# Performance work log

Measured on AMD Instinct MI355X. Metric: run time of the kernel, lower is better.

Reference implementation:

```python
import jax, jax.numpy as jnp
import numpy as np

H, DK, NF, DC, B, T = 8, 64, 512, 256, 8, 1024

def setup_inputs() -> dict:
    key = jax.random.key(0)
    ks = jax.random.split(key, 16)
    s = lambda fan_in: 1.0 / np.sqrt(fan_in)
    return {
        "x": jax.random.normal(ks[0], (B, T, NF), jnp.float32),
        "cond": jax.random.normal(ks[1], (B, T, DC), jnp.float32),
        "pos_k": jax.random.normal(ks[2], (T, T, DK), jnp.float32),
        "mask": jax.random.randint(ks[3], (B, T, T), 0, 2, jnp.int32),
        "ln_gamma": jnp.ones((NF,), jnp.float32),
        "ln_beta": jnp.zeros((NF,), jnp.float32),
        "Wq": jax.random.uniform(ks[4], (NF, NF), jnp.float32, -s(NF), s(NF)),
        "bq": jax.random.uniform(ks[5], (NF,), jnp.float32, -s(NF), s(NF)),
        "Wk": jax.random.uniform(ks[6], (NF, NF), jnp.float32, -s(NF), s(NF)),
        "bk": jax.random.uniform(ks[7], (NF,), jnp.float32, -s(NF), s(NF)),
        "Wv": jax.random.uniform(ks[8], (NF, NF), jnp.float32, -s(NF), s(NF)),
        "bv": jax.random.uniform(ks[9], (NF,), jnp.float32, -s(NF), s(NF)),
        "Wo": jax.random.uniform(ks[10], (NF, NF), jnp.float32, -s(NF), s(NF)),
        "bo": jax.random.uniform(ks[11], (NF,), jnp.float32, -s(NF), s(NF)),
        "Wc": jax.random.uniform(ks[12], (DC, NF), jnp.float32, -s(DC), s(DC)),
        "bc": jax.random.uniform(ks[13], (NF,), jnp.float32, -s(DC), s(DC)),
    }

def reference(x, cond, pos_k, mask, ln_gamma, ln_beta, Wq, bq, Wk, bk, Wv, bv, Wo, bo, Wc, bc):
    # LayerNorm over features (eps matches torch default)
    mu = jnp.mean(x, axis=-1, keepdims=True)
    var = jnp.mean(jnp.square(x - mu), axis=-1, keepdims=True)
    xn = (x - mu) * jax.lax.rsqrt(var + 1e-5) * ln_gamma + ln_beta
    # projections; query comes from conditioning signal
    q = ((cond @ Wc + bc) @ Wq + bq).reshape(B, T, H, DK)
    k = (xn @ Wk + bk).reshape(B, T, H, DK)
    v = (xn @ Wv + bv).reshape(B, T, H, DK)
    # content scores + relative-position bias (matmul-trick equivalent)
    A = jnp.einsum('bthd,bshd->bhts', q, k)
    Bbias = jnp.einsum('bthd,tsd->bhts', q, pos_k)
    scores = (A + Bbias) / np.sqrt(DK)
    m0 = (mask == 0)[:, None, :, :]  # (B,1,T,T) True where masked
    min_val = jnp.finfo(scores.dtype).min
    scores = jnp.where(m0, min_val, scores)
    attn = jnp.where(m0, 0.0, jax.nn.softmax(scores, axis=-1))
    out = jnp.einsum('bhts,bshd->bthd', attn, v).reshape(B, T, NF)
    return out @ Wo + bo
```

## Files before the change

### kernel.cpp

```cpp
#include <hip/hip_runtime.h>

#define Bb 8
#define Tt 1024
#define Hh 8
#define DKk 64
#define NFf 512
#define DCc 256

typedef _Float16 v2h __attribute__((ext_vector_type(2)));
typedef _Float16 v4h __attribute__((ext_vector_type(4)));
typedef _Float16 v8h __attribute__((ext_vector_type(8)));
typedef float    v4f __attribute__((ext_vector_type(4)));
typedef float    v16f __attribute__((ext_vector_type(16)));

#define MFMA32(a,b,c) __builtin_amdgcn_mfma_f32_16x16x32_f16((a),(b),(c),0,0,0)
#define MFMA3216(a,b,c) __builtin_amdgcn_mfma_f32_32x32x16_f16((a),(b),(c),0,0,0)

#define SCQ 0.1803368801111f

__device__ inline void st8(_Float16* dst, v8h x){
    *(v4h*)dst     = __builtin_shufflevector(x,x,0,1,2,3);
    *(v4h*)(dst+4) = __builtin_shufflevector(x,x,4,5,6,7);
}

__device__ inline v8h cvt8(float4 a, float4 b){
    v8h r;
    r[0]=(_Float16)a.x; r[1]=(_Float16)a.y; r[2]=(_Float16)a.z; r[3]=(_Float16)a.w;
    r[4]=(_Float16)b.x; r[5]=(_Float16)b.y; r[6]=(_Float16)b.z; r[7]=(_Float16)b.w;
    return r;
}

__device__ inline int swz(int r, int c){ return (r*64 + c) ^ ((r&7)<<3); }

__global__ __launch_bounds__(256) void k_ln(const float* __restrict__ x,
                                            const float* __restrict__ g,
                                            const float* __restrict__ be,
                                            _Float16* __restrict__ xn){
    int row = blockIdx.x; int tid = threadIdx.x;
    const float* xr = x + (size_t)row*512;
    float2 v = reinterpret_cast<const float2*>(xr)[tid];
    float s = v.x + v.y, sq = v.x*v.x + v.y*v.y;
    for (int off=32; off; off>>=1){ s += __shfl_down(s, off); sq += __shfl_down(sq, off); }
    __shared__ float ws_[4], wq_[4];
    __shared__ float mu_s, rs_s;
    int wid = tid>>6, lid = tid&63;
    if (lid==0){ ws_[wid]=s; wq_[wid]=sq; }
    __syncthreads();
    if (tid==0){
        float S=0,Q=0;
        for(int i=0;i<4;i++){S+=ws_[i];Q+=wq_[i];}
        float mu = S*(1.f/512.f);
        float var = Q*(1.f/512.f)-mu*mu;
        mu_s=mu; rs_s=rsqrtf(var+1e-5f);
    }
    __syncthreads();
    float mu=mu_s, rs=rs_s;
    float2 gv = reinterpret_cast<const float2*>(g)[tid];
    float2 bv = reinterpret_cast<const float2*>(be)[tid];
    v2h o; o[0] = (_Float16)((v.x-mu)*rs*gv.x + bv.x);
           o[1] = (_Float16)((v.y-mu)*rs*gv.y + bv.y);
    reinterpret_cast<v2h*>(xn + (size_t)row*512)[tid] = o;
}

__global__ __launch_bounds__(256) void k_wT4(const float* __restrict__ W0,
                                             const float* __restrict__ W1,
                                             const float* __restrict__ W2,
                                             const float* __restrict__ W3,
                                             _Float16* __restrict__ T0,
                                             _Float16* __restrict__ T1,
                                             _Float16* __restrict__ T2,
                                             _Float16* __restrict__ T3){
    const float* W = (blockIdx.z==0)?W0:(blockIdx.z==1)?W1:(blockIdx.z==2)?W2:W3;
    _Float16*  WT = (blockIdx.z==0)?T0:(blockIdx.z==1)?T1:(blockIdx.z==2)?T2:T3;
    __shared__ float tile[64][65];
    int bx = blockIdx.x*64, by = blockIdx.y*64;
    int tid = threadIdx.x, c = tid&63;
    for (int r = tid>>6; r<64; r+=4) tile[r][c] = W[(size_t)(by+r)*512 + bx + c];
    __syncthreads();
    for (int n = tid>>6; n<64; n+=4) WT[(size_t)(bx+n)*512 + by + c] = (_Float16)tile[c][n];
}

__global__ __launch_bounds__(256) void k_h16(const float* __restrict__ src,
                                             _Float16* __restrict__ dst){
    int i = (blockIdx.x*256 + threadIdx.x)*8;
    float4 a = *(const float4*)(src+i);
    float4 b = *(const float4*)(src+i+4);
    *(v8h*)(dst+i) = cvt8(a,b);
}

__global__ __launch_bounds__(512) void k_bcqp(const float* __restrict__ bc,
                                              const float* __restrict__ Wq,
                                              float* __restrict__ bcq){
    int j = threadIdx.x; int m0 = blockIdx.x*16;
    float a = 0.f;
    #pragma unroll
    for (int m=0;m<16;m++) a += bc[m0+m]*Wq[(size_t)(m0+m)*512 + j];
    atomicAdd(&bcq[j], a);
}

template<typename AT, typename CT, bool QB>
__global__ __launch_bounds__(512) void k_gemm(const AT* __restrict__ A,
                                              const _Float16* __restrict__ WT,
                                              const float* __restrict__ bias,
                                              CT* __restrict__ C,
                                              int M, int N, int K,
                                              float scale,
                                              _Float16* __restrict__ qbT){
    __shared__ _Float16 Al[2][128*64];
    __shared__ _Float16 Wl[2][128*64];
    int tid = threadIdx.x, l = tid&63, w = tid>>6;
    int l15 = l&15, lq = l>>4;
    int wr = w>>2, wc = w&3;
    int m0 = blockIdx.y*128, n0 = blockIdx.x*128;
    v4f acc[4][2] = {};
    float bv[2];
    #pragma unroll
    for (int bc=0;bc<2;++bc) bv[bc] = bias[n0 + wc*32 + bc*16 + l15];
    int srow = tid>>2, sseg = (tid&3)*16;
    const AT* arow = A + (size_t)(m0+srow)*K + sseg;
    const _Float16* wrow = WT + (size_t)(n0+srow)*K + sseg;
    int NT = K>>6;

    v8h pa0, pa1, pw0, pw1;
    if constexpr (sizeof(AT)==4){
        const float* s = (const float*)arow;
        pa0 = cvt8(*(const float4*)s,     *(const float4*)(s+4));
        pa1 = cvt8(*(const float4*)(s+8), *(const float4*)(s+12));
    } else {
        pa0 = *(const v8h*)arow; pa1 = *(const v8h*)(arow+8);
    }
    pw0 = *(const v8h*)wrow; pw1 = *(const v8h*)(wrow+8);
    st8(&Al[0][swz(srow,sseg)], pa0); st8(&Al[0][swz(srow,sseg+8)], pa1);
    st8(&Wl[0][swz(srow,sseg)], pw0); st8(&Wl[0][swz(srow,sseg+8)], pw1);
    __syncthreads();

    for (int kt=0; kt<NT; ++kt){
        int cur = kt&1;
        if (kt < NT-1){
            int k0 = (kt+1)<<6;
            if constexpr (sizeof(AT)==4){
                const float* s = (const float*)arow + k0;
                pa0 = cvt8(*(const float4*)s,     *(const float4*)(s+4));
                pa1 = cvt8(*(const float4*)(s+8), *(const float4*)(s+12));
            } else {
                pa0 = *(const v8h*)(arow + k0); pa1 = *(const v8h*)(arow + k0 + 8);
            }
            pw0 = *(const v8h*)(wrow + k0); pw1 = *(const v8h*)(wrow + k0 + 8);
        }
        #pragma unroll
        for (int kk=0; kk<2; ++kk){
            v8h af[4], bf[2];
            #pragma unroll
            for (int ar=0;ar<4;++ar) af[ar] = *(v8h*)&Al[cur][swz(wr*64+ar*16+l15, kk*32+lq*8)];
            #pragma unroll
            for (int bc=0;bc<2;++bc) bf[bc] = *(v8h*)&Wl[cur][swz(wc*32+bc*16+l15, kk*32+lq*8)];
            #pragma unroll
            for (int ar=0;ar<4;++ar)
                #pragma unroll
                for (int bc=0;bc<2;++bc)
                    acc[ar][bc] = MFMA32(af[ar], bf[bc], acc[ar][bc]);
        }
        if (kt < NT-1){
            st8(&Al[cur^1][swz(srow,sseg)], pa0); st8(&Al[cur^1][swz(srow,sseg+8)], pa1);
            st8(&Wl[cur^1][swz(srow,sseg)], pw0); st8(&Wl[cur^1][swz(srow,sseg+8)], pw1);
        }
        __syncthreads();
    }
    #pragma unroll
    for (int ar=0;ar<4;++ar){
        #pragma unroll
        for (int bc=0;bc<2;++bc){
            #pragma unroll
            for (int i=0;i<4;++i){
                int row = m0 + wr*64 + ar*16 + lq*4 + i;
                int col = n0 + wc*32 + bc*16 + l15;
                float vf = (acc[ar][bc][i] + bv[bc])*scale;
                C[(size_t)row*N + col] = (CT)vf;
                if constexpr (QB){
                    int bI = row>>10, t = row&1023;
                    qbT[((size_t)t<<12) + (bI<<9) + col] = (_Float16)vf;
                }
            }
        }
    }
}

__global__ __launch_bounds__(512) void k_gemmkv(const _Float16* __restrict__ A,
                                                const _Float16* __restrict__ WTk,
                                                const _Float16* __restrict__ WTv,
                                                const float* __restrict__ bk,
                                                const float* __restrict__ bv,
                                                _Float16* __restrict__ Ck,
                                                _Float16* __restrict__ Cv){
    __shared__ _Float16 Al[2][128*64];
    __shared__ _Float16 Wkl[2][128*64];
    __shared__ _Float16 Wvl[2][128*64];
    int tid = threadIdx.x, l = tid&63, w = tid>>6;
    int l15 = l&15, lq = l>>4;
    int wr = w>>2, wc = w&3;
    int m0 = blockIdx.y*128, n0 = blockIdx.x*128;
    v4f ack[4][2] = {}, acv[4][2] = {};
    float bkr[2], bvr[2];
    #pragma unroll
    for (int bc=0;bc<2;++bc){ bkr[bc] = bk[n0 + wc*32 + bc*16 + l15]; bvr[bc] = bv[n0 + wc*32 + bc*16 + l15]; }
    int srow = tid>>2, sseg = (tid&3)*16;
    const _Float16* arow = A   + (size_t)(m0+srow)*512 + sseg;
    const _Float16* krow = WTk + (size_t)(n0+srow)*512 + sseg;
    const _Float16* vrow = WTv + (size_t)(n0+srow)*512 + sseg;

    v8h pa0,pa1,pk0,pk1,pv0,pv1;
    pa0 = *(const v8h*)arow; pa1 = *(const v8h*)(arow+8);
    pk0 = *(const v8h*)krow; pk1 = *(const v8h*)(krow+8);
    pv0 = *(const v8h*)vrow; pv1 = *(const v8h*)(vrow+8);
    st8(&Al[0][swz(srow,sseg)],  pa0); st8(&Al[0][swz(srow,sseg+8)],  pa1);
    st8(&Wkl[0][swz(srow,sseg)], pk0); st8(&Wkl[0][swz(srow,sseg+8)], pk1);
    st8(&Wvl[0][swz(srow,sseg)], pv0); st8(&Wvl[0][swz(srow,sseg+8)], pv1);
    __syncthreads();

    for (int kt=0; kt<8; ++kt){
        int cur = kt&1;
        if (kt < 7){
            int k0 = (kt+1)<<6;
            pa0 = *(const v8h*)(arow+k0); pa1 = *(const v8h*)(arow+k0+8);
            pk0 = *(const v8h*)(krow+k0); pk1 = *(const v8h*)(krow+k0+8);
            pv0 = *(const v8h*)(vrow+k0); pv1 = *(const v8h*)(vrow+k0+8);
        }
        #pragma unroll
        for (int kk=0; kk<2; ++kk){
            v8h af[4], kf[2], vf[2];
            #pragma unroll
            for (int ar=0;ar<4;++ar) af[ar] = *(v8h*)&Al[cur][swz(wr*64+ar*16+l15, kk*32+lq*8)];
            #pragma unroll
            for (int bc=0;bc<2;++bc){
                kf[bc] = *(v8h*)&Wkl[cur][swz(wc*32+bc*16+l15, kk*32+lq*8)];
                vf[bc] = *(v8h*)&Wvl[cur][swz(wc*32+bc*16+l15, kk*32+lq*8)];
            }
            #pragma unroll
            for (int ar=0;ar<4;++ar)
                #pragma unroll
                for (int bc=0;bc<2;++bc){
                    ack[ar][bc] = MFMA32(af[ar], kf[bc], ack[ar][bc]);
                    acv[ar][bc] = MFMA32(af[ar], vf[bc], acv[ar][bc]);
                }
        }
        if (kt < 7){
            st8(&Al[cur^1][swz(srow,sseg)],  pa0); st8(&Al[cur^1][swz(srow,sseg+8)],  pa1);
            st8(&Wkl[cur^1][swz(srow,sseg)], pk0); st8(&Wkl[cur^1][swz(srow,sseg+8)], pk1);
            st8(&Wvl[cur^1][swz(srow,sseg)], pv0); st8(&Wvl[cur^1][swz(srow,sseg+8)], pv1);
        }
        __syncthreads();
    }
    #pragma unroll
    for (int ar=0;ar<4;++ar){
        #pragma unroll
        for (int bc=0;bc<2;++bc){
            #pragma unroll
            for (int i=0;i<4;++i){
                int row = m0 + wr*64 + ar*16 + lq*4 + i;
                int col = n0 + wc*32 + bc*16 + l15;
                Ck[(size_t)row*512 + col] = (_Float16)(ack[ar][bc][i] + bkr[bc]);
                Cv[(size_t)row*512 + col] = (_Float16)(acv[ar][bc][i] + bvr[bc]);
            }
        }
    }
}

__global__ __launch_bounds__(256) void k_bias(const _Float16* __restrict__ qb,
                                              const float* __restrict__ posk,
                                              const int* __restrict__ mask,
                                              _Float16* __restrict__ Sb){
    __shared__ _Float16 Pl[2][64*64];
    __shared__ _Float16 Ol[2][64*72];
    int t = blockIdx.x >> 1, sh = blockIdx.x & 1;
    int tid = threadIdx.x, l = tid&63, w = tid>>6;
    int l31 = l&31, hi = l>>5;
    int g = w & 1, sg = w >> 1;
    v8h aa[4];
    const _Float16* qbt = qb + ((size_t)t<<12);
    #pragma unroll
    for (int k0=0;k0<4;++k0)
        aa[k0] = *(const v8h*)(qbt + (g*32 + l31)*64 + k0*16 + hi*8);

    const float* pkt = posk + ((size_t)t<<16);
    int sbase = sh*512;
    int lrow = (l>>4), lcol = (l&15)*4;

    v4f pf[4];
    #pragma unroll
    for (int j=0;j<4;++j)
        pf[j] = *(const v4f*)(pkt + (size_t)(sbase + w*16 + j*4 + lrow)*64 + lcol);

    int obh = tid>>2;
    int osl = (tid&3)*16;
    int ob  = obh>>3;
    const int* mbase = mask + (((size_t)(ob*Tt + t))<<10);
    _Float16* sbb = Sb + (((size_t)(t*64 + obh))<<10);

    #pragma unroll
    for (int j=0;j<4;++j){
        v4h hv; hv[0]=(_Float16)pf[j][0]; hv[1]=(_Float16)pf[j][1];
                hv[2]=(_Float16)pf[j][2]; hv[3]=(_Float16)pf[j][3];
        *(v4h*)&Pl[0][swz(w*16 + j*4 + lrow, lcol)] = hv;
    }
    __syncthreads();

    for (int sc=0; sc<8; ++sc){
        int cur = sc&1;
        int s0 = sbase + sc*64;
        if (sc < 7){
            #pragma unroll
            for (int j=0;j<4;++j)
                pf[j] = *(const v4f*)(pkt + (size_t)(s0 + 64 + w*16 + j*4 + lrow)*64 + lcol);
        }
        int4 mq[4];
        #pragma unroll
        for (int j=0;j<4;++j)
            mq[j] = *(const int4*)(mbase + s0 + osl + j*4);
        v8h bfr[4];
        #pragma unroll
        for (int k0=0;k0<4;++k0)
            bfr[k0] = *(v8h*)&Pl[cur][swz(sg*32 + l31, k0*16 + hi*8)];
        v16f acc = {};
        #pragma unroll
        for (int k0=0;k0<4;++k0) acc = MFMA3216(aa[k0], bfr[k0], acc);
        #pragma unroll
        for (int r=0;r<16;++r){
            int bh = g*32 + (r&3) + 4*hi + 8*(r>>2);
            Ol[cur][bh*72 + sg*32 + l31] = (_Float16)acc[r];
        }
        if (sc < 7){
            #pragma unroll
            for (int j=0;j<4;++j){
                v4h hv; hv[0]=(_Float16)pf[j][0]; hv[1]=(_Float16)pf[j][1];
                        hv[2]=(_Float16)pf[j][2]; hv[3]=(_Float16)pf[j][3];
                *(v4h*)&Pl[cur^1][swz(w*16 + j*4 + lrow, lcol)] = hv;
            }
        }
        __syncthreads();
        v8h o0 = *(v8h*)&Ol[cur][obh*72 + osl];
        v8h o1 = *(v8h*)&Ol[cur][obh*72 + osl + 8];
        const _Float16 NEG = (_Float16)(-30000.f);
        int mm[16] = {mq[0].x,mq[0].y,mq[0].z,mq[0].w, mq[1].x,mq[1].y,mq[1].z,mq[1].w,
                      mq[2].x,mq[2].y,mq[2].z,mq[2].w, mq[3].x,mq[3].y,mq[3].z,mq[3].w};
        #pragma unroll
        for (int j=0;j<8;++j){ if(!mm[j]) o0[j]=NEG; if(!mm[8+j]) o1[j]=NEG; }
        *(v8h*)(sbb + s0 + osl)     = o0;
        *(v8h*)(sbb + s0 + osl + 8) = o1;
    }
}

__global__ __launch_bounds__(512) void k_flash(const _Float16* __restrict__ qs,
                                               const _Float16* __restrict__ kbuf,
                                               const _Float16* __restrict__ vbuf,
                                               const _Float16* __restrict__ Sb,
                                               _Float16* __restrict__ ao){
    __shared__ _Float16 Kl[64*64];
    __shared__ _Float16 Vt[64*64];
    __shared__ _Float16 Bl[128*64];
    int bh = blockIdx.x; int b = bh>>3, h = bh&7;
    int t0 = blockIdx.y*128;
    int tid = threadIdx.x, l = tid&63, w = tid>>6, l15 = l&15, lq = l>>4;

    v8h qa[2];
    #pragma unroll
    for (int u=0;u<2;++u)
        qa[u] = *(const v8h*)(qs + ((size_t)(b*Tt + t0 + w*16 + l15))*NFf + h*DKk + u*32 + lq*8);

    v4f O[4] = {};
    float m_l = -1e30f, l_l = 0.f;

    int kr = tid>>3, kseg = (tid&7)*8;
    int vs = tid&63, vd0 = (tid>>6)*8;
    int br = tid>>2, bhf = (tid&3)*16;
    const _Float16* kbase = kbuf + ((size_t)(b*Tt + kr))*NFf + h*DKk + kseg;
    const _Float16* vbase = vbuf + ((size_t)(b*Tt + vs))*NFf + h*DKk + vd0;
    const _Float16* bbase = Sb + (((size_t)((t0+br)*64 + bh))<<10) + bhf;

    v8h pk = *(const v8h*)kbase;
    v8h pv = *(const v8h*)vbase;
    v8h pb0 = *(const v8h*)bbase;
    v8h pb1 = *((const v8h*)bbase + 1);

    for (int sc=0; sc<16; ++sc){
        st8(&Kl[swz(kr, kseg)], pk);
        #pragma unroll
        for (int j=0;j<8;j++) Vt[swz(vd0+j, vs)] = pv[j];
        st8(&Bl[swz(br, bhf)],   pb0);
        st8(&Bl[swz(br, bhf+8)], pb1);
        __syncthreads();
        if (sc < 15){
            size_t soff = (size_t)(sc+1)*64;
            pk  = *(const v8h*)(kbase + soff*NFf);
            pv  = *(const v8h*)(vbase + soff*NFf);
            pb0 = *(const v8h*)(bbase + soff);
            pb1 = *((const v8h*)(bbase + soff) + 1);
        }

        v4f sv[4];
        #pragma unroll
        for (int nt=0; nt<4; ++nt){
            v8h kb0 = *(v8h*)&Kl[swz(nt*16+l15, lq*8)];
            v8h kb1 = *(v8h*)&Kl[swz(nt*16+l15, 32+lq*8)];
            v4f a = {};
            a = MFMA32(kb0, qa[0], a);
            a = MFMA32(kb1, qa[1], a);
            v4h bl4 = *(v4h*)&Bl[swz(w*16 + l15, nt*16 + lq*4)];
            #pragma unroll
            for (int i=0;i<4;i++) a[i] += (float)bl4[i];
            sv[nt] = a;
        }
        float mx = fmaxf(fmaxf(fmaxf(sv[0][0],sv[0][1]),fmaxf(sv[0][2],sv[0][3])),
                   fmaxf(fmaxf(fmaxf(sv[1][0],sv[1][1]),fmaxf(sv[1][2],sv[1][3])),
                   fmaxf(fmaxf(fmaxf(sv[2][0],sv[2][1]),fmaxf(sv[2][2],sv[2][3])),
                         fmaxf(fmaxf(sv[3][0],sv[3][1]),fmaxf(sv[3][2],sv[3][3])))));
        mx = fmaxf(mx, __shfl_xor(mx,16));
        mx = fmaxf(mx, __shfl_xor(mx,32));
        float mn = fmaxf(m_l, mx);
        if (__any(mn - m_l > 0.f)){
            float rsc = exp2f(m_l - mn);
            m_l = mn; l_l *= rsc;
            float rscB[4];
            #pragma unroll
            for (int i=0;i<4;i++) rscB[i] = __shfl(rsc, lq*4+i);
            #pragma unroll
            for (int nt=0; nt<4; ++nt)
                #pragma unroll
                for (int i=0;i<4;i++) O[nt][i] *= rscB[i];
        }
        float ps = 0.f;
        #pragma unroll
        for (int nt=0; nt<4; ++nt){
            v4h ph;
            #pragma unroll
            for (int i=0;i<4;i++){
                float p = exp2f(sv[nt][i] - m_l);
                ph[i] = (_Float16)p;
                ps += p;
            }
            *(v4h*)&Bl[swz(w*16 + l15, nt*16 + lq*4)] = ph;
        }
        ps += __shfl_xor(ps,16);
        ps += __shfl_xor(ps,32);
        l_l += ps;
        {
            v8h pa0 = *(v8h*)&Bl[swz(w*16+l15, lq*8)];
            v8h pa1 = *(v8h*)&Bl[swz(w*16+l15, 32+lq*8)];
            #pragma unroll
            for (int nt=0; nt<4; ++nt){
                v8h vb0 = *(v8h*)&Vt[swz(nt*16+l15, lq*8)];
                v8h vb1 = *(v8h*)&Vt[swz(nt*16+l15, 32+lq*8)];
                O[nt] = MFMA32(pa0, vb0, O[nt]);
                O[nt] = MFMA32(pa1, vb1, O[nt]);
            }
        }
        __syncthreads();
    }

    float rl = (l_l > 0.f) ? 1.f/l_l : 0.f;
    float rlB[4];
    #pragma unroll
    for (int i=0;i<4;i++) rlB[i] = __shfl(rl, lq*4+i);
    #pragma unroll
    for (int i=0;i<4;i++){
        int row = t0 + w*16 + lq*4 + i;
        #pragma unroll
        for (int nt=0; nt<4; ++nt)
            ao[((size_t)(b*Tt + row))*NFf + h*DKk + nt*16 + l15] = (_Float16)(O[nt][i]*rlB[i]);
    }
}

extern "C" void kernel_launch(void* const* d_in, const int* in_sizes, int n_in,
                              void* d_out, int out_size, void* d_ws, size_t ws_size,
                              hipStream_t stream) {
    const float* x       = (const float*)d_in[0];
    const float* cond    = (const float*)d_in[1];
    const float* pos_k   = (const float*)d_in[2];
    const int*   mask    = (const int*)  d_in[3];
    const float* ln_g    = (const float*)d_in[4];
    const float* ln_b    = (const float*)d_in[5];
    const float* Wq      = (const float*)d_in[6];
    const float* bq      = (const float*)d_in[7];
    const float* Wk      = (const float*)d_in[8];
    const float* bk      = (const float*)d_in[9];
    const float* Wv      = (const float*)d_in[10];
    const float* bv      = (const float*)d_in[11];
    const float* Wo      = (const float*)d_in[12];
    const float* bo      = (const float*)d_in[13];
    const float* Wc      = (const float*)d_in[14];
    const float* bc      = (const float*)d_in[15];
    float* out = (float*)d_out;

    char* base = (char*)d_ws;
    const size_t OFF_S    = 0;
    const size_t OFF_XN   = 134217728;
    const size_t OFF_Q    = OFF_XN  + 8388608;
    const size_t OFF_QB   = OFF_Q   + 8388608;
    const size_t OFF_K    = OFF_QB  + 8388608;
    const size_t OFF_V    = OFF_K   + 8388608;
    const size_t OFF_AO   = OFF_V   + 8388608;
    const size_t OFF_WKT  = OFF_AO  + 8388608;
    const size_t OFF_WVT  = OFF_WKT + 524288;
    const size_t OFF_WOT  = OFF_WVT + 524288;
    const size_t OFF_WQT  = OFF_WOT + 524288;
    const size_t OFF_WCH  = OFF_WQT + 524288;
    const size_t OFF_WCQT = OFF_WCH + 262144;
    const size_t OFF_BCQ  = OFF_WCQT + 262144;
    const size_t OFF_ZERO = OFF_BCQ + 2048;

    _Float16* xn    = (_Float16*)(base + OFF_XN);
    _Float16* qbuf  = (_Float16*)(base + OFF_Q);
    _Float16* qb    = (_Float16*)(base + OFF_QB);
    _Float16* kb    = (_Float16*)(base + OFF_K);
    _Float16* vb    = (_Float16*)(base + OFF_V);
    _Float16* ao    = (_Float16*)(base + OFF_AO);
    _Float16* Sb    = (_Float16*)(base + OFF_S);
    _Float16* WkT   = (_Float16*)(base + OFF_WKT);
    _Float16* WvT   = (_Float16*)(base + OFF_WVT);
    _Float16* WoT   = (_Float16*)(base + OFF_WOT);
    _Float16* WqT   = (_Float16*)(base + OFF_WQT);
    _Float16* WcH   = (_Float16*)(base + OFF_WCH);
    _Float16* wcqT  = (_Float16*)(base + OFF_WCQT);
    float*    bcq   = (float*)(base + OFF_BCQ);
    float*    zero  = (float*)(base + OFF_ZERO);

    hipMemsetAsync(zero, 0, 1024, stream);
    hipMemcpyAsync(bcq, bq, 2048, hipMemcpyDeviceToDevice, stream);

    k_ln<<<dim3(Bb*Tt), dim3(256), 0, stream>>>(x, ln_g, ln_b, xn);
    k_wT4<<<dim3(8,8,4), dim3(256), 0, stream>>>(Wk, Wv, Wo, Wq, WkT, WvT, WoT, WqT);
    k_h16<<<dim3(64), dim3(256), 0, stream>>>(Wc, WcH);
    k_bcqp<<<dim3(16), dim3(512), 0, stream>>>(bc, Wq, bcq);

    k_gemm<_Float16,_Float16,false><<<dim3(2,4), dim3(512), 0, stream>>>(WqT, WcH, zero, wcqT, 512, 256, 512, 1.f, nullptr);

    k_gemm<float,_Float16,true><<<dim3(4,64), dim3(512), 0, stream>>>(cond, wcqT, bcq, qbuf, Bb*Tt, 512, 256, SCQ, qb);
    k_gemmkv<<<dim3(4,64), dim3(512), 0, stream>>>(xn, WkT, WvT, bk, bv, kb, vb);

    k_bias<<<dim3(2048), dim3(256), 0, stream>>>(qb, pos_k, mask, Sb);
    k_flash<<<dim3(64,8), dim3(512), 0, stream>>>(qbuf, kb, vb, Sb, ao);

    k_gemm<_Float16,float,false><<<dim3(4,64), dim3(512), 0, stream>>>(ao, WoT, bo, out, Bb*Tt, 512, 512, 1.f, nullptr);
}
```

Baseline: 225.1 us.

## Double-buffer flash attention LDS tiles and fuse weight prep kernels

Flash attention now keeps two LDS buffers for the K, V and bias tiles. The next tile is stored into the alternate buffer after the PV MFMAs, so each iteration needs one barrier instead of two. Weight transposes, the Wc fp16 conversion, the zero buffer init and the bias copy are merged into one prep kernel, replacing the separate memset/memcpy calls and extra launches. In exchange the attention kernel's shared memory use doubles, which may lower occupancy.

```diff
diff --git a/kernel.cpp b/kernel.cpp
--- a/kernel.cpp
+++ b/kernel.cpp
@@ -62,30 +62,39 @@
     reinterpret_cast<v2h*>(xn + (size_t)row*512)[tid] = o;
 }
 
-__global__ __launch_bounds__(256) void k_wT4(const float* __restrict__ W0,
-                                             const float* __restrict__ W1,
-                                             const float* __restrict__ W2,
-                                             const float* __restrict__ W3,
-                                             _Float16* __restrict__ T0,
-                                             _Float16* __restrict__ T1,
-                                             _Float16* __restrict__ T2,
-                                             _Float16* __restrict__ T3){
-    const float* W = (blockIdx.z==0)?W0:(blockIdx.z==1)?W1:(blockIdx.z==2)?W2:W3;
-    _Float16*  WT = (blockIdx.z==0)?T0:(blockIdx.z==1)?T1:(blockIdx.z==2)?T2:T3;
+__global__ __launch_bounds__(256) void k_prep(const float* __restrict__ Wk,
+                                              const float* __restrict__ Wv,
+                                              const float* __restrict__ Wo,
+                                              const float* __restrict__ Wq,
+                                              _Float16* __restrict__ WkT,
+                                              _Float16* __restrict__ WvT,
+                                              _Float16* __restrict__ WoT,
+                                              _Float16* __restrict__ WqT,
+                                              const float* __restrict__ Wc,
+                                              _Float16* __restrict__ WcH,
+                                              const float* __restrict__ bq,
+                                              float* __restrict__ bcq,
+                                              float* __restrict__ zero){
     __shared__ float tile[64][65];
-    int bx = blockIdx.x*64, by = blockIdx.y*64;
-    int tid = threadIdx.x, c = tid&63;
-    for (int r = tid>>6; r<64; r+=4) tile[r][c] = W[(size_t)(by+r)*512 + bx + c];
-    __syncthreads();
-    for (int n = tid>>6; n<64; n+=4) WT[(size_t)(bx+n)*512 + by + c] = (_Float16)tile[c][n];
-}
-
-__global__ __launch_bounds__(256) void k_h16(const float* __restrict__ src,
-                                             _Float16* __restrict__ dst){
-    int i = (blockIdx.x*256 + threadIdx.x)*8;
-    float4 a = *(const float4*)(src+i);
-    float4 b = *(const float4*)(src+i+4);
-    *(v8h*)(dst+i) = cvt8(a,b);
+    int z = blockIdx.z;
+    int tid = threadIdx.x;
+    if (z < 4){
+        const float* W = (z==0)?Wk:(z==1)?Wv:(z==2)?Wo:Wq;
+        _Float16*  WT = (z==0)?WkT:(z==1)?WvT:(z==2)?WoT:WqT;
+        int bx = blockIdx.x*64, by = blockIdx.y*64;
+        int c = tid&63;
+        for (int r = tid>>6; r<64; r+=4) tile[r][c] = W[(size_t)(by+r)*512 + bx + c];
+        __syncthreads();
+        for (int n = tid>>6; n<64; n+=4) WT[(size_t)(bx+n)*512 + by + c] = (_Float16)tile[c][n];
+    } else {
+        int idx = blockIdx.y*8 + blockIdx.x;
+        int i = (idx*256 + tid)*8;
+        float4 a = *(const float4*)(Wc+i);
+        float4 b2 = *(const float4*)(Wc+i+4);
+        *(v8h*)(WcH+i) = cvt8(a,b2);
+        if (idx == 0) zero[tid] = 0.f;
+        if (idx == 1){ bcq[tid] = bq[tid]; bcq[tid+256] = bq[tid+256]; }
+    }
 }
 
 __global__ __launch_bounds__(512) void k_bcqp(const float* __restrict__ bc,
@@ -354,9 +363,9 @@
                                                const _Float16* __restrict__ vbuf,
                                                const _Float16* __restrict__ Sb,
                                                _Float16* __restrict__ ao){
-    __shared__ _Float16 Kl[64*64];
-    __shared__ _Float16 Vt[64*64];
-    __shared__ _Float16 Bl[128*64];
+    __shared__ _Float16 Kl[2][64*64];
+    __shared__ _Float16 Vt[2][64*64];
+    __shared__ _Float16 Bl[2][128*64];
     int bh = blockIdx.x; int b = bh>>3, h = bh&7;
     int t0 = blockIdx.y*128;
     int tid = threadIdx.x, l = tid&63, w = tid>>6, l15 = l&15, lq = l>>4;
@@ -380,14 +389,15 @@
     v8h pv = *(const v8h*)vbase;
     v8h pb0 = *(const v8h*)bbase;
     v8h pb1 = *((const v8h*)bbase + 1);
+    st8(&Kl[0][swz(kr, kseg)], pk);
+    #pragma unroll
+    for (int j=0;j<8;j++) Vt[0][swz(vd0+j, vs)] = pv[j];
+    st8(&Bl[0][swz(br, bhf)],   pb0);
+    st8(&Bl[0][swz(br, bhf+8)], pb1);
+    __syncthreads();
 
     for (int sc=0; sc<16; ++sc){
-        st8(&Kl[swz(kr, kseg)], pk);
-        #pragma unroll
-        for (int j=0;j<8;j++) Vt[swz(vd0+j, vs)] = pv[j];
-        st8(&Bl[swz(br, bhf)],   pb0);
-        st8(&Bl[swz(br, bhf+8)], pb1);
-        __syncthreads();
+        int cur = sc&1;
         if (sc < 15){
             size_t soff = (size_t)(sc+1)*64;
             pk  = *(const v8h*)(kbase + soff*NFf);
@@ -399,12 +409,12 @@
         v4f sv[4];
         #pragma unroll
         for (int nt=0; nt<4; ++nt){
-            v8h kb0 = *(v8h*)&Kl[swz(nt*16+l15, lq*8)];
-            v8h kb1 = *(v8h*)&Kl[swz(nt*16+l15, 32+lq*8)];
+            v8h kb0 = *(v8h*)&Kl[cur][swz(nt*16+l15, lq*8)];
+            v8h kb1 = *(v8h*)&Kl[cur][swz(nt*16+l15, 32+lq*8)];
             v4f a = {};
             a = MFMA32(kb0, qa[0], a);
             a = MFMA32(kb1, qa[1], a);
-            v4h bl4 = *(v4h*)&Bl[swz(w*16 + l15, nt*16 + lq*4)];
+            v4h bl4 = *(v4h*)&Bl[cur][swz(w*16 + l15, nt*16 + lq*4)];
             #pragma unroll
             for (int i=0;i<4;i++) a[i] += (float)bl4[i];
             sv[nt] = a;
@@ -437,21 +447,28 @@
                 ph[i] = (_Float16)p;
                 ps += p;
             }
-            *(v4h*)&Bl[swz(w*16 + l15, nt*16 + lq*4)] = ph;
+            *(v4h*)&Bl[cur][swz(w*16 + l15, nt*16 + lq*4)] = ph;
         }
         ps += __shfl_xor(ps,16);
         ps += __shfl_xor(ps,32);
         l_l += ps;
         {
-            v8h pa0 = *(v8h*)&Bl[swz(w*16+l15, lq*8)];
-            v8h pa1 = *(v8h*)&Bl[swz(w*16+l15, 32+lq*8)];
+            v8h pa0 = *(v8h*)&Bl[cur][swz(w*16+l15, lq*8)];
+            v8h pa1 = *(v8h*)&Bl[cur][swz(w*16+l15, 32+lq*8)];
             #pragma unroll
             for (int nt=0; nt<4; ++nt){
-                v8h vb0 = *(v8h*)&Vt[swz(nt*16+l15, lq*8)];
-                v8h vb1 = *(v8h*)&Vt[swz(nt*16+l15, 32+lq*8)];
+                v8h vb0 = *(v8h*)&Vt[cur][swz(nt*16+l15, lq*8)];
+                v8h vb1 = *(v8h*)&Vt[cur][swz(nt*16+l15, 32+lq*8)];
                 O[nt] = MFMA32(pa0, vb0, O[nt]);
                 O[nt] = MFMA32(pa1, vb1, O[nt]);
             }
+        }
+        if (sc < 15){
+            st8(&Kl[cur^1][swz(kr, kseg)], pk);
+            #pragma unroll
+            for (int j=0;j<8;j++) Vt[cur^1][swz(vd0+j, vs)] = pv[j];
+            st8(&Bl[cur^1][swz(br, bhf)],   pb0);
+            st8(&Bl[cur^1][swz(br, bhf+8)], pb1);
         }
         __syncthreads();
     }
@@ -523,12 +540,8 @@
     float*    bcq   = (float*)(base + OFF_BCQ);
     float*    zero  = (float*)(base + OFF_ZERO);
 
-    hipMemsetAsync(zero, 0, 1024, stream);
-    hipMemcpyAsync(bcq, bq, 2048, hipMemcpyDeviceToDevice, stream);
-
     k_ln<<<dim3(Bb*Tt), dim3(256), 0, stream>>>(x, ln_g, ln_b, xn);
-    k_wT4<<<dim3(8,8,4), dim3(256), 0, stream>>>(Wk, Wv, Wo, Wq, WkT, WvT, WoT, WqT);
-    k_h16<<<dim3(64), dim3(256), 0, stream>>>(Wc, WcH);
+    k_prep<<<dim3(8,8,5), dim3(256), 0, stream>>>(Wk, Wv, Wo, Wq, WkT, WvT, WoT, WqT, Wc, WcH, bq, bcq, zero);
     k_bcqp<<<dim3(16), dim3(512), 0, stream>>>(bc, Wq, bcq);
 
     k_gemm<_Float16,_Float16,false><<<dim3(2,4), dim3(512), 0, stream>>>(WqT, WcH, zero, wcqT, 512, 256, 512, 1.f, nullptr);
```

After: 217.2 us. -3.5%, faster.
